# Optimization experiments

Hardware: AMD Instinct MI355X
Metric: run time of the kernel (lower is better)

Reference implementation:

```python
import jax, jax.numpy as jnp
import numpy as np

N = 50000        # num nodes
E = 800000       # num edges (no self loops by construction)
D = 128          # in_features == out_features
NE = 4           # num_envs
EPS = 1e-8
STDV = 1.0 / np.sqrt(D)


def setup_inputs() -> dict:
    key = jax.random.key(0)
    k = jax.random.split(key, 6)
    x = jax.random.normal(k[0], (N, D), jnp.float32)
    row = jax.random.randint(k[1], (E,), 0, N, dtype=jnp.int32)
    off = jax.random.randint(k[2], (E,), 1, N, dtype=jnp.int32)
    col = (row + off) % N  # guarantees no self loops (matches remove_self_loops)
    adj = jnp.stack([row, col])
    env_weights = jax.random.uniform(k[3], (N, NE), jnp.float32)
    weights = jax.random.uniform(k[4], (NE, D, D), jnp.float32, -STDV, STDV)
    a = jax.random.normal(k[5], (NE, 2 * D, 1), jnp.float32) * np.sqrt(2.0 / (2 * D + 1)) * 1.414
    return {"x": x, "adj": adj, "env_weights": env_weights, "weights": weights, "a": a}


def reference(x, adj, env_weights, weights, a):
    n = x.shape[0]
    f = weights.shape[-1]
    loops = jnp.arange(n, dtype=adj.dtype)
    src = jnp.concatenate([adj[0], loops])  # add_self_loops
    dst = jnp.concatenate([adj[1], loops])
    # per-env projected features: [NE, N, F]
    h = jnp.einsum('nd,edf->enf', x, weights)
    # attention logits: cat(h[src], h[dst]) @ a  ==  h[src]@a1 + h[dst]@a2
    a1 = a[:, :f, 0]   # [NE, F]
    a2 = a[:, f:, 0]   # [NE, F]
    s_src = jnp.einsum('enf,ef->en', h, a1)
    s_dst = jnp.einsum('enf,ef->en', h, a2)
    logits = jax.nn.leaky_relu(s_src[:, src] + s_dst[:, dst], 0.01)  # [NE, Etot]
    # global per-env max subtraction (as in the torch code: max over all edges)
    e = jnp.exp(logits - jnp.max(logits, axis=1, keepdims=True))
    def agg(ek, hk):
        # specialspmm: out[src] += ek * hk[dst]; denom via ones vector
        denom = jax.ops.segment_sum(ek, src, num_segments=n) + EPS          # [N]
        num = jax.ops.segment_sum(ek[:, None] * hk[dst], src, num_segments=n)  # [N, F]
        return num / denom[:, None]
    out_env = jax.vmap(agg)(e, h)  # [NE, N, F]
    out = jnp.einsum('ne,enf->nf', env_weights, out_env)
    return out + x  # residual
```

## Files before the change

kernel.cpp:

```cpp
#include <hip/hip_runtime.h>

#define N_NODES 50000
#define N_EDGES 800000
#define D_FEAT  128
#define NE_ENV  4
#define EPS_F   1e-8f
#define M_CONST 4.0f
#define SCAN_NB 196
#define NB_BUCKET 391
#define BINA_EPT 16

typedef __attribute__((ext_vector_type(8))) short bf16x8;
typedef __attribute__((ext_vector_type(4))) float floatx4;

static __device__ __forceinline__ unsigned short f2bf(float v) {
    union { float f; unsigned int u; } c; c.f = v;
    unsigned int u = c.u;
    u += 0x7fffu + ((u >> 16) & 1u);
    return (unsigned short)(u >> 16);
}

static __device__ __forceinline__ float2 bf2f(unsigned int v) {
    float2 r;
    r.x = __uint_as_float(v << 16);
    r.y = __uint_as_float(v & 0xffff0000u);
    return r;
}

static __device__ __forceinline__ float lrelu_exp(float z) {
    float lk = z > 0.f ? z : 0.01f * z;
    return __expf(lk - M_CONST);
}

__global__ __launch_bounds__(256) void k_setup(const float* __restrict__ weights, const float* __restrict__ a,
        float* __restrict__ b, unsigned short* __restrict__ wsw,
        const int* __restrict__ row, int* __restrict__ counts) {
    int blk = blockIdx.x;
    if (blk < 128) {
        int wave = threadIdx.x >> 6, lane = threadIdx.x & 63;
        int t = blk * 4 + wave;
        int e = t >> 7, d = t & 127;
        float2 w2 = ((const float2*)(weights + e * 16384 + d * 128))[lane];
        float2 a1 = ((const float2*)(a + e * 256))[lane];
        float2 a2 = ((const float2*)(a + e * 256 + 128))[lane];
        float p1 = w2.x * a1.x + w2.y * a1.y;
        float p2 = w2.x * a2.x + w2.y * a2.y;
#pragma unroll
        for (int off = 32; off > 0; off >>= 1) {
            p1 += __shfl_xor(p1, off, 64);
            p2 += __shfl_xor(p2, off, 64);
        }
        if (lane == 0) {
            b[e * 128 + d] = p1;
            b[512 + e * 128 + d] = p2;
        }
    } else if (blk < 384) {
        int idx = (blk - 128) * 256 + threadIdx.x;
        int j = idx & 7;
        int l = (idx >> 3) & 63;
        int t = (idx >> 9) & 7;
        int s = idx >> 12;
        int k = s * 32 + (l >> 4) * 8 + j;
        int f = t * 16 + (l & 15);
        int e = k >> 7, d = k & 127;
        wsw[idx] = f2bf(weights[e * 16384 + d * 128 + f]);
    } else {
        int k = (blk - 384) * 256 + threadIdx.x;
        if (k < N_EDGES) atomicAdd(&counts[row[k]], 1);
    }
}

__global__ __launch_bounds__(256) void k_s(const float* __restrict__ x, const float* __restrict__ b,
        float* __restrict__ s_src, float* __restrict__ s_dst, unsigned short* __restrict__ xbf) {
    int wave = threadIdx.x >> 6, lane = threadIdx.x & 63;
    int gw = blockIdx.x * 4 + wave;
    if (gw >= 3125) return;
    int quad = lane >> 4, lm = lane & 15;
    int base = gw * 16;

    floatx4 acc = (floatx4){0.f, 0.f, 0.f, 0.f};
    const float* xrow = x + (size_t)(base + lm) * 128 + quad * 8;
    unsigned short* xbrow = xbf + (size_t)(base + lm) * 128 + quad * 8;

#pragma unroll
    for (int s = 0; s < 4; ++s) {
        float4 lo = *(const float4*)(xrow + s * 32);
        float4 hi = *(const float4*)(xrow + s * 32 + 4);
        bf16x8 af;
        af[0] = (short)f2bf(lo.x); af[1] = (short)f2bf(lo.y);
        af[2] = (short)f2bf(lo.z); af[3] = (short)f2bf(lo.w);
        af[4] = (short)f2bf(hi.x); af[5] = (short)f2bf(hi.y);
        af[6] = (short)f2bf(hi.z); af[7] = (short)f2bf(hi.w);
        *(bf16x8*)(xbrow + s * 32) = af;

        bf16x8 bfv = (bf16x8){0, 0, 0, 0, 0, 0, 0, 0};
        if (lm < 8) {
            const float* bp = b + lm * 128 + s * 32 + quad * 8;
            float4 b0 = *(const float4*)bp;
            float4 b1 = *(const float4*)(bp + 4);
            bfv[0] = (short)f2bf(b0.x); bfv[1] = (short)f2bf(b0.y);
            bfv[2] = (short)f2bf(b0.z); bfv[3] = (short)f2bf(b0.w);
            bfv[4] = (short)f2bf(b1.x); bfv[5] = (short)f2bf(b1.y);
            bfv[6] = (short)f2bf(b1.z); bfv[7] = (short)f2bf(b1.w);
        }
        acc = __builtin_amdgcn_mfma_f32_16x16x32_bf16(af, bfv, acc, 0, 0, 0);
    }
    if (lm < 8) {
        float* dstp = (lm < 4) ? (s_src + (size_t)(base + quad * 4) * 4 + lm)
                               : (s_dst + (size_t)(base + quad * 4) * 4 + (lm - 4));
#pragma unroll
        for (int r = 0; r < 4; ++r) dstp[r * 4] = acc[r];
    }
}

__global__ void k_scan_a(const int* __restrict__ counts, int* __restrict__ partial) {
    __shared__ int sm[256];
    int idx = blockIdx.x * 256 + threadIdx.x;
    sm[threadIdx.x] = (idx < N_NODES) ? counts[idx] : 0;
    __syncthreads();
    for (int s = 128; s > 0; s >>= 1) {
        if (threadIdx.x < s) sm[threadIdx.x] += sm[threadIdx.x + s];
        __syncthreads();
    }
    if (threadIdx.x == 0) partial[blockIdx.x] = sm[0];
}

__global__ void k_scan_b(const int* __restrict__ partial, int* __restrict__ chunk_off) {
    __shared__ int sm[256];
    int t = threadIdx.x;
    int v = (t < SCAN_NB) ? partial[t] : 0;
    sm[t] = v;
    __syncthreads();
    for (int s2 = 1; s2 < 256; s2 <<= 1) {
        int add = (t >= s2) ? sm[t - s2] : 0;
        __syncthreads();
        sm[t] += add;
        __syncthreads();
    }
    chunk_off[t] = sm[t] - v;
}

__global__ void k_scan_c(const int* __restrict__ counts, const int* __restrict__ chunk_off,
                         int* __restrict__ offsets, int* __restrict__ bcur) {
    __shared__ int sm[256];
    int t = threadIdx.x;
    int idx = blockIdx.x * 256 + t;
    int v = (idx < N_NODES) ? counts[idx] : 0;
    sm[t] = v;
    __syncthreads();
    for (int s2 = 1; s2 < 256; s2 <<= 1) {
        int add = (t >= s2) ? sm[t - s2] : 0;
        __syncthreads();
        sm[t] += add;
        __syncthreads();
    }
    if (idx < N_NODES) {
        int excl = chunk_off[blockIdx.x] + sm[t] - v;
        offsets[idx] = excl;
        if ((idx & 127) == 0) bcur[idx >> 7] = excl;
    }
    if (idx == 0) offsets[N_NODES] = N_EDGES;
}

__global__ __launch_bounds__(256) void k_binA(const int* __restrict__ row, const int* __restrict__ col,
        int* __restrict__ bcur, unsigned int* __restrict__ binned) {
    __shared__ int cnt[NB_BUCKET];
    __shared__ int base[NB_BUCKET];
    int t = threadIdx.x;
    for (int b = t; b < NB_BUCKET; b += 256) cnt[b] = 0;
    __syncthreads();
    unsigned int pk[BINA_EPT];
    int ebase = blockIdx.x * (256 * BINA_EPT) + t;
#pragma unroll
    for (int j = 0; j < BINA_EPT; ++j) {
        int k = ebase + j * 256;
        pk[j] = 0xffffffffu;
        if (k < N_EDGES) {
            unsigned int s = (unsigned int)row[k];
            unsigned int d = (unsigned int)col[k];
            pk[j] = (s << 16) | d;
            atomicAdd(&cnt[s >> 7], 1);
        }
    }
    __syncthreads();
    for (int b = t; b < NB_BUCKET; b += 256) {
        int c = cnt[b];
        base[b] = c ? atomicAdd(&bcur[b], c) : 0;
        cnt[b] = 0;
    }
    __syncthreads();
#pragma unroll
    for (int j = 0; j < BINA_EPT; ++j) {
        if (pk[j] != 0xffffffffu) {
            int b = pk[j] >> 23;
            int off = atomicAdd(&cnt[b], 1);
            binned[base[b] + off] = pk[j];
        }
    }
}

__global__ __launch_bounds__(256) void k_binB(const unsigned int* __restrict__ binned,
        const int* __restrict__ offsets,
        const float* __restrict__ s_src, const float* __restrict__ s_dst,
        int* __restrict__ sorted_dst, float4* __restrict__ w_sorted) {
    __shared__ int cur[128];
    int b = blockIdx.x;
    int nb = b << 7;
    int nc = min(128, N_NODES - nb);
    int t = threadIdx.x;
    if (t < nc) cur[t] = offsets[nb + t];
    __syncthreads();
    int ebeg = offsets[nb];
    int eend = offsets[nb + nc];
    for (int i = ebeg + t; i < eend; i += 256) {
        unsigned int pk = binned[i];
        int s = (int)(pk >> 16), d = (int)(pk & 0xffffu);
        float4 a4 = *(const float4*)(s_src + s * 4);
        float4 b4 = *(const float4*)(s_dst + d * 4);
        float4 w;
        w.x = lrelu_exp(a4.x + b4.x);
        w.y = lrelu_exp(a4.y + b4.y);
        w.z = lrelu_exp(a4.z + b4.z);
        w.w = lrelu_exp(a4.w + b4.w);
        int pos = atomicAdd(&cur[s - nb], 1);
        sorted_dst[pos] = d;
        w_sorted[pos] = w;
    }
}

__global__ __launch_bounds__(256) void k_agg(const unsigned int* __restrict__ xb,
        const float* __restrict__ s_src, const float* __restrict__ s_dst,
        const int* __restrict__ offsets, const int* __restrict__ sorted_dst,
        const float4* __restrict__ w_sorted, const float* __restrict__ env_w,
        unsigned short* __restrict__ Gp) {
    int wave = threadIdx.x >> 6, lane = threadIdx.x & 63;
    int n = blockIdx.x * 4 + wave;
    if (n >= N_NODES) return;

    float den[4], ax[4], ay[4];

    {
        float4 sa = *(const float4*)(s_src + n * 4);
        float4 sb = *(const float4*)(s_dst + n * 4);
        float ws[4] = { lrelu_exp(sa.x + sb.x), lrelu_exp(sa.y + sb.y),
                        lrelu_exp(sa.z + sb.z), lrelu_exp(sa.w + sb.w) };
        float2 xv = bf2f(xb[(size_t)n * 64 + lane]);
#pragma unroll
        for (int e = 0; e < 4; ++e) {
            den[e] = ws[e]; ax[e] = ws[e] * xv.x; ay[e] = ws[e] * xv.y;
        }
    }

    int beg = __builtin_amdgcn_readfirstlane(offsets[n]);
    int end = __builtin_amdgcn_readfirstlane(offsets[n + 1]);
    int i = beg;
    for (; i + 3 < end; i += 4) {
        int d0 = sorted_dst[i],     d1 = sorted_dst[i + 1];
        int d2 = sorted_dst[i + 2], d3 = sorted_dst[i + 3];
        float4 w0 = w_sorted[i],     w1 = w_sorted[i + 1];
        float4 w2 = w_sorted[i + 2], w3 = w_sorted[i + 3];
        unsigned int v0 = xb[(size_t)d0 * 64 + lane];
        unsigned int v1 = xb[(size_t)d1 * 64 + lane];
        unsigned int v2 = xb[(size_t)d2 * 64 + lane];
        unsigned int v3 = xb[(size_t)d3 * 64 + lane];
        float2 x0 = bf2f(v0), x1 = bf2f(v1), x2v = bf2f(v2), x3 = bf2f(v3);
        den[0] += (w0.x + w1.x) + (w2.x + w3.x);
        den[1] += (w0.y + w1.y) + (w2.y + w3.y);
        den[2] += (w0.z + w1.z) + (w2.z + w3.z);
        den[3] += (w0.w + w1.w) + (w2.w + w3.w);
        ax[0] += w0.x * x0.x + w1.x * x1.x + w2.x * x2v.x + w3.x * x3.x;
        ay[0] += w0.x * x0.y + w1.x * x1.y + w2.x * x2v.y + w3.x * x3.y;
        ax[1] += w0.y * x0.x + w1.y * x1.x + w2.y * x2v.x + w3.y * x3.x;
        ay[1] += w0.y * x0.y + w1.y * x1.y + w2.y * x2v.y + w3.y * x3.y;
        ax[2] += w0.z * x0.x + w1.z * x1.x + w2.z * x2v.x + w3.z * x3.x;
        ay[2] += w0.z * x0.y + w1.z * x1.y + w2.z * x2v.y + w3.z * x3.y;
        ax[3] += w0.w * x0.x + w1.w * x1.x + w2.w * x2v.x + w3.w * x3.x;
        ay[3] += w0.w * x0.y + w1.w * x1.y + w2.w * x2v.y + w3.w * x3.y;
    }
    for (; i < end; ++i) {
        int d0 = sorted_dst[i];
        float4 w0 = w_sorted[i];
        float2 x0 = bf2f(xb[(size_t)d0 * 64 + lane]);
        den[0] += w0.x; den[1] += w0.y; den[2] += w0.z; den[3] += w0.w;
        ax[0] += w0.x * x0.x; ay[0] += w0.x * x0.y;
        ax[1] += w0.y * x0.x; ay[1] += w0.y * x0.y;
        ax[2] += w0.z * x0.x; ay[2] += w0.z * x0.y;
        ax[3] += w0.w * x0.x; ay[3] += w0.w * x0.y;
    }

    float4 ewt = *(const float4*)(env_w + n * 4);
    float ewv[4] = { ewt.x, ewt.y, ewt.z, ewt.w };
    unsigned int* grow = (unsigned int*)(Gp + (size_t)n * 512);
#pragma unroll
    for (int e = 0; e < 4; ++e) {
        float sc = ewv[e] / (den[e] + EPS_F);
        unsigned int lo = f2bf(sc * ax[e]);
        unsigned int hi = f2bf(sc * ay[e]);
        grow[e * 64 + lane] = (hi << 16) | lo;
    }
}

__global__ __launch_bounds__(256) void k_gemm(const unsigned short* __restrict__ Gp,
        const unsigned short* __restrict__ Wsw,
        const float* __restrict__ x, float* __restrict__ out) {
    int wave = threadIdx.x >> 6, lane = threadIdx.x & 63;
    int gw = blockIdx.x * 4 + wave;
    if (gw >= 3125) return;
    int quad = lane >> 4, lm = lane & 15;
    int m = gw * 16 + lm;

    floatx4 acc[8];
#pragma unroll
    for (int t = 0; t < 8; ++t) acc[t] = (floatx4){0.f, 0.f, 0.f, 0.f};

    const unsigned short* Arow = Gp + (size_t)m * 512 + quad * 8;
#pragma unroll
    for (int s = 0; s < 16; ++s) {
        bf16x8 af = *(const bf16x8*)(Arow + s * 32);
#pragma unroll
        for (int t = 0; t < 8; ++t) {
            bf16x8 bfv = *(const bf16x8*)(Wsw + (((s * 8 + t) * 64 + lane) * 8));
            acc[t] = __builtin_amdgcn_mfma_f32_16x16x32_bf16(af, bfv, acc[t], 0, 0, 0);
        }
    }
    int row_base = gw * 16 + quad * 4;
#pragma unroll
    for (int t = 0; t < 8; ++t) {
        int colc = t * 16 + lm;
#pragma unroll
        for (int r = 0; r < 4; ++r) {
            int rowi = row_base + r;
            out[rowi * 128 + colc] = acc[t][r] + x[rowi * 128 + colc];
        }
    }
}

extern "C" void kernel_launch(void* const* d_in, const int* in_sizes, int n_in,
                              void* d_out, int out_size, void* d_ws, size_t ws_size,
                              hipStream_t stream) {
    const float* x       = (const float*)d_in[0];
    const int*   adj     = (const int*)d_in[1];
    const int*   row     = adj;
    const int*   col     = adj + N_EDGES;
    const float* env_w   = (const float*)d_in[2];
    const float* weights = (const float*)d_in[3];
    const float* a       = (const float*)d_in[4];
    float* out = (float*)d_out;

    char* ws = (char*)d_ws;
    size_t off = 0;
    auto alloc = [&](size_t bytes) -> char* {
        char* p = ws + off;
        off += (bytes + 255) & ~(size_t)255;
        return p;
    };
    float* b          = (float*)alloc(1024 * 4);
    float* s_src      = (float*)alloc((size_t)N_NODES * 4 * 4);
    float* s_dst      = (float*)alloc((size_t)N_NODES * 4 * 4);
    int*   counts     = (int*)alloc((size_t)N_NODES * 4);
    int*   offsets    = (int*)alloc((size_t)(N_NODES + 1) * 4);
    int*   partial    = (int*)alloc(256 * 4);
    int*   chunk_off  = (int*)alloc(256 * 4);
    int*   bcur       = (int*)alloc(512 * 4);
    unsigned int* binned = (unsigned int*)alloc((size_t)N_EDGES * 4);
    int*   sorted_dst = (int*)alloc((size_t)N_EDGES * 4);
    float4* w_sorted  = (float4*)alloc((size_t)N_EDGES * 16);
    unsigned short* wsw = (unsigned short*)alloc(65536 * 2);
    unsigned short* xbf = (unsigned short*)alloc((size_t)N_NODES * 128 * 2);
    unsigned short* Gp  = (unsigned short*)alloc((size_t)N_NODES * 512 * 2);

    hipMemsetAsync(counts, 0, (size_t)N_NODES * 4, stream);
    k_setup<<<3509, 256, 0, stream>>>(weights, a, b, wsw, row, counts);
    k_s<<<782, 256, 0, stream>>>(x, b, s_src, s_dst, xbf);
    k_scan_a<<<SCAN_NB, 256, 0, stream>>>(counts, partial);
    k_scan_b<<<1, 256, 0, stream>>>(partial, chunk_off);
    k_scan_c<<<SCAN_NB, 256, 0, stream>>>(counts, chunk_off, offsets, bcur);
    k_binA<<<196, 256, 0, stream>>>(row, col, bcur, binned);
    k_binB<<<NB_BUCKET, 256, 0, stream>>>(binned, offsets, s_src, s_dst, sorted_dst, w_sorted);
    k_agg<<<12500, 256, 0, stream>>>((const unsigned int*)xbf, s_src, s_dst, offsets, sorted_dst, w_sorted, env_w, Gp);
    k_gemm<<<782, 256, 0, stream>>>(Gp, wsw, x, out);
}
```

Before: 231.6 us.

## Fold softmax normalization into binning and drop separate scan kernels

Removes the three-kernel prefix scan by computing per-bucket sums in an extra k_s block and scanning node offsets locally in k_binB. k_binB now accumulates per-node denominators in shared memory and emits edge coefficients already scaled by env weight over denominator, plus a self-loop coefficient. This lets k_agg drop its denominator and env-weight work and use packed float2 FMAs. The GEMM residual reads bf16 x instead of fp32 x to cut traffic, at the cost of residual precision and a second pass over edges in binB.

```diff
diff --git a/kernel.cpp b/kernel.cpp
--- a/kernel.cpp
+++ b/kernel.cpp
@@ -6,12 +6,12 @@
 #define NE_ENV  4
 #define EPS_F   1e-8f
 #define M_CONST 4.0f
-#define SCAN_NB 196
 #define NB_BUCKET 391
 #define BINA_EPT 16
 
 typedef __attribute__((ext_vector_type(8))) short bf16x8;
 typedef __attribute__((ext_vector_type(4))) float floatx4;
+typedef __attribute__((ext_vector_type(2))) float f2v;
 
 static __device__ __forceinline__ unsigned short f2bf(float v) {
     union { float f; unsigned int u; } c; c.f = v;
@@ -20,8 +20,8 @@
     return (unsigned short)(u >> 16);
 }
 
-static __device__ __forceinline__ float2 bf2f(unsigned int v) {
-    float2 r;
+static __device__ __forceinline__ f2v bf2f2(unsigned int v) {
+    f2v r;
     r.x = __uint_as_float(v << 16);
     r.y = __uint_as_float(v & 0xffff0000u);
     return r;
@@ -71,7 +71,45 @@
 }
 
 __global__ __launch_bounds__(256) void k_s(const float* __restrict__ x, const float* __restrict__ b,
-        float* __restrict__ s_src, float* __restrict__ s_dst, unsigned short* __restrict__ xbf) {
+        float* __restrict__ s_src, float* __restrict__ s_dst, unsigned short* __restrict__ xbf,
+        const int* __restrict__ counts, int* __restrict__ bcur, int* __restrict__ bbase) {
+    __shared__ int bsum[512];
+    if (blockIdx.x == 782) {
+        int t = threadIdx.x;
+        int o0 = 0, o1 = 0;
+        {
+            int nb = t << 7;
+            int n = min(128, N_NODES - nb);
+            for (int j = 0; j < n; ++j) o0 += counts[nb + j];
+            bsum[t] = o0;
+        }
+        {
+            int b1 = t + 256;
+            if (b1 < NB_BUCKET) {
+                int nb = b1 << 7;
+                int n = min(128, N_NODES - nb);
+                for (int j = 0; j < n; ++j) o1 += counts[nb + j];
+            }
+            bsum[t + 256] = o1;
+        }
+        __syncthreads();
+        for (int st = 1; st < 512; st <<= 1) {
+            int v0 = (t >= st) ? bsum[t - st] : 0;
+            int v1 = (t + 256 >= st) ? bsum[t + 256 - st] : 0;
+            __syncthreads();
+            bsum[t] += v0;
+            bsum[t + 256] += v1;
+            __syncthreads();
+        }
+        int e0 = bsum[t] - o0;
+        bcur[t] = e0; bbase[t] = e0;
+        int b1 = t + 256;
+        if (b1 < NB_BUCKET) {
+            int e1 = bsum[b1] - o1;
+            bcur[b1] = e1; bbase[b1] = e1;
+        }
+        return;
+    }
     int wave = threadIdx.x >> 6, lane = threadIdx.x & 63;
     int gw = blockIdx.x * 4 + wave;
     if (gw >= 3125) return;
@@ -113,55 +151,6 @@
     }
 }
 
-__global__ void k_scan_a(const int* __restrict__ counts, int* __restrict__ partial) {
-    __shared__ int sm[256];
-    int idx = blockIdx.x * 256 + threadIdx.x;
-    sm[threadIdx.x] = (idx < N_NODES) ? counts[idx] : 0;
-    __syncthreads();
-    for (int s = 128; s > 0; s >>= 1) {
-        if (threadIdx.x < s) sm[threadIdx.x] += sm[threadIdx.x + s];
-        __syncthreads();
-    }
-    if (threadIdx.x == 0) partial[blockIdx.x] = sm[0];
-}
-
-__global__ void k_scan_b(const int* __restrict__ partial, int* __restrict__ chunk_off) {
-    __shared__ int sm[256];
-    int t = threadIdx.x;
-    int v = (t < SCAN_NB) ? partial[t] : 0;
-    sm[t] = v;
-    __syncthreads();
-    for (int s2 = 1; s2 < 256; s2 <<= 1) {
-        int add = (t >= s2) ? sm[t - s2] : 0;
-        __syncthreads();
-        sm[t] += add;
-        __syncthreads();
-    }
-    chunk_off[t] = sm[t] - v;
-}
-
-__global__ void k_scan_c(const int* __restrict__ counts, const int* __restrict__ chunk_off,
-                         int* __restrict__ offsets, int* __restrict__ bcur) {
-    __shared__ int sm[256];
-    int t = threadIdx.x;
-    int idx = blockIdx.x * 256 + t;
-    int v = (idx < N_NODES) ? counts[idx] : 0;
-    sm[t] = v;
-    __syncthreads();
-    for (int s2 = 1; s2 < 256; s2 <<= 1) {
-        int add = (t >= s2) ? sm[t - s2] : 0;
-        __syncthreads();
-        sm[t] += add;
-        __syncthreads();
-    }
-    if (idx < N_NODES) {
-        int excl = chunk_off[blockIdx.x] + sm[t] - v;
-        offsets[idx] = excl;
-        if ((idx & 127) == 0) bcur[idx >> 7] = excl;
-    }
-    if (idx == 0) offsets[N_NODES] = N_EDGES;
-}
-
 __global__ __launch_bounds__(256) void k_binA(const int* __restrict__ row, const int* __restrict__ col,
         int* __restrict__ bcur, unsigned int* __restrict__ binned) {
     __shared__ int cnt[NB_BUCKET];
@@ -200,55 +189,100 @@
 }
 
 __global__ __launch_bounds__(256) void k_binB(const unsigned int* __restrict__ binned,
-        const int* __restrict__ offsets,
+        const int* __restrict__ counts, const int* __restrict__ bbase,
         const float* __restrict__ s_src, const float* __restrict__ s_dst,
-        int* __restrict__ sorted_dst, float4* __restrict__ w_sorted) {
+        const float* __restrict__ env_w,
+        int* __restrict__ offsets, int* __restrict__ sorted_dst,
+        float4* __restrict__ c_sorted, float4* __restrict__ cself) {
+    __shared__ int sc[128];
     __shared__ int cur[128];
+    __shared__ float denm[128][4];
     int b = blockIdx.x;
     int nb = b << 7;
     int nc = min(128, N_NODES - nb);
     int t = threadIdx.x;
-    if (t < nc) cur[t] = offsets[nb + t];
-    __syncthreads();
-    int ebeg = offsets[nb];
-    int eend = offsets[nb + nc];
+    int myc = 0;
+    if (t < nc) myc = counts[nb + t];
+    if (t < 128) sc[t] = myc;
+    __syncthreads();
+    for (int st = 1; st < 128; st <<= 1) {
+        int v = 0;
+        if (t < 128 && t >= st) v = sc[t - st];
+        __syncthreads();
+        if (t < 128) sc[t] += v;
+        __syncthreads();
+    }
+    int base = bbase[b];
+    float4 wself = {0.f, 0.f, 0.f, 0.f};
+    if (t < nc) {
+        int excl = base + sc[t] - myc;
+        offsets[nb + t] = excl;
+        cur[t] = excl;
+        float4 sa = *(const float4*)(s_src + (size_t)(nb + t) * 4);
+        float4 sb = *(const float4*)(s_dst + (size_t)(nb + t) * 4);
+        wself.x = lrelu_exp(sa.x + sb.x);
+        wself.y = lrelu_exp(sa.y + sb.y);
+        wself.z = lrelu_exp(sa.z + sb.z);
+        wself.w = lrelu_exp(sa.w + sb.w);
+        denm[t][0] = wself.x; denm[t][1] = wself.y;
+        denm[t][2] = wself.z; denm[t][3] = wself.w;
+    }
+    int tot = sc[127];
+    __syncthreads();
+    int ebeg = base, eend = base + tot;
     for (int i = ebeg + t; i < eend; i += 256) {
         unsigned int pk = binned[i];
         int s = (int)(pk >> 16), d = (int)(pk & 0xffffu);
-        float4 a4 = *(const float4*)(s_src + s * 4);
-        float4 b4 = *(const float4*)(s_dst + d * 4);
-        float4 w;
-        w.x = lrelu_exp(a4.x + b4.x);
-        w.y = lrelu_exp(a4.y + b4.y);
-        w.z = lrelu_exp(a4.z + b4.z);
-        w.w = lrelu_exp(a4.w + b4.w);
-        int pos = atomicAdd(&cur[s - nb], 1);
+        float4 a4 = *(const float4*)(s_src + (size_t)s * 4);
+        float4 b4 = *(const float4*)(s_dst + (size_t)d * 4);
+        int ls = s - nb;
+        atomicAdd(&denm[ls][0], lrelu_exp(a4.x + b4.x));
+        atomicAdd(&denm[ls][1], lrelu_exp(a4.y + b4.y));
+        atomicAdd(&denm[ls][2], lrelu_exp(a4.z + b4.z));
+        atomicAdd(&denm[ls][3], lrelu_exp(a4.w + b4.w));
+    }
+    __syncthreads();
+    if (t < nc) {
+        float4 ew = *(const float4*)(env_w + (size_t)(nb + t) * 4);
+        float m0 = ew.x / (denm[t][0] + EPS_F);
+        float m1 = ew.y / (denm[t][1] + EPS_F);
+        float m2 = ew.z / (denm[t][2] + EPS_F);
+        float m3 = ew.w / (denm[t][3] + EPS_F);
+        denm[t][0] = m0; denm[t][1] = m1; denm[t][2] = m2; denm[t][3] = m3;
+        cself[nb + t] = make_float4(m0 * wself.x, m1 * wself.y, m2 * wself.z, m3 * wself.w);
+    }
+    __syncthreads();
+    for (int i = ebeg + t; i < eend; i += 256) {
+        unsigned int pk = binned[i];
+        int s = (int)(pk >> 16), d = (int)(pk & 0xffffu);
+        int ls = s - nb;
+        float4 a4 = *(const float4*)(s_src + (size_t)s * 4);
+        float4 b4 = *(const float4*)(s_dst + (size_t)d * 4);
+        float4 c;
+        c.x = denm[ls][0] * lrelu_exp(a4.x + b4.x);
+        c.y = denm[ls][1] * lrelu_exp(a4.y + b4.y);
+        c.z = denm[ls][2] * lrelu_exp(a4.z + b4.z);
+        c.w = denm[ls][3] * lrelu_exp(a4.w + b4.w);
+        int pos = atomicAdd(&cur[ls], 1);
         sorted_dst[pos] = d;
-        w_sorted[pos] = w;
-    }
-}
-
-__global__ __launch_bounds__(256) void k_agg(const unsigned int* __restrict__ xb,
-        const float* __restrict__ s_src, const float* __restrict__ s_dst,
+        c_sorted[pos] = c;
+    }
+    if (b == NB_BUCKET - 1 && t == 0) offsets[N_NODES] = N_EDGES;
+}
+
+__global__ __launch_bounds__(256, 8) void k_agg(const unsigned int* __restrict__ xb,
         const int* __restrict__ offsets, const int* __restrict__ sorted_dst,
-        const float4* __restrict__ w_sorted, const float* __restrict__ env_w,
+        const float4* __restrict__ c_sorted, const float4* __restrict__ cself,
         unsigned short* __restrict__ Gp) {
     int wave = threadIdx.x >> 6, lane = threadIdx.x & 63;
     int n = blockIdx.x * 4 + wave;
     if (n >= N_NODES) return;
 
-    float den[4], ax[4], ay[4];
-
+    f2v a0, a1, a2, a3;
     {
-        float4 sa = *(const float4*)(s_src + n * 4);
-        float4 sb = *(const float4*)(s_dst + n * 4);
-        float ws[4] = { lrelu_exp(sa.x + sb.x), lrelu_exp(sa.y + sb.y),
-                        lrelu_exp(sa.z + sb.z), lrelu_exp(sa.w + sb.w) };
-        float2 xv = bf2f(xb[(size_t)n * 64 + lane]);
-#pragma unroll
-        for (int e = 0; e < 4; ++e) {
-            den[e] = ws[e]; ax[e] = ws[e] * xv.x; ay[e] = ws[e] * xv.y;
-        }
+        float4 cs = cself[n];
+        f2v xv = bf2f2(xb[(size_t)n * 64 + lane]);
+        a0 = cs.x * xv; a1 = cs.y * xv; a2 = cs.z * xv; a3 = cs.w * xv;
     }
 
     int beg = __builtin_amdgcn_readfirstlane(offsets[n]);
@@ -257,52 +291,35 @@
     for (; i + 3 < end; i += 4) {
         int d0 = sorted_dst[i],     d1 = sorted_dst[i + 1];
         int d2 = sorted_dst[i + 2], d3 = sorted_dst[i + 3];
-        float4 w0 = w_sorted[i],     w1 = w_sorted[i + 1];
-        float4 w2 = w_sorted[i + 2], w3 = w_sorted[i + 3];
+        float4 c0 = c_sorted[i],     c1 = c_sorted[i + 1];
+        float4 c2 = c_sorted[i + 2], c3 = c_sorted[i + 3];
         unsigned int v0 = xb[(size_t)d0 * 64 + lane];
         unsigned int v1 = xb[(size_t)d1 * 64 + lane];
         unsigned int v2 = xb[(size_t)d2 * 64 + lane];
         unsigned int v3 = xb[(size_t)d3 * 64 + lane];
-        float2 x0 = bf2f(v0), x1 = bf2f(v1), x2v = bf2f(v2), x3 = bf2f(v3);
-        den[0] += (w0.x + w1.x) + (w2.x + w3.x);
-        den[1] += (w0.y + w1.y) + (w2.y + w3.y);
-        den[2] += (w0.z + w1.z) + (w2.z + w3.z);
-        den[3] += (w0.w + w1.w) + (w2.w + w3.w);
-        ax[0] += w0.x * x0.x + w1.x * x1.x + w2.x * x2v.x + w3.x * x3.x;
-        ay[0] += w0.x * x0.y + w1.x * x1.y + w2.x * x2v.y + w3.x * x3.y;
-        ax[1] += w0.y * x0.x + w1.y * x1.x + w2.y * x2v.x + w3.y * x3.x;
-        ay[1] += w0.y * x0.y + w1.y * x1.y + w2.y * x2v.y + w3.y * x3.y;
-        ax[2] += w0.z * x0.x + w1.z * x1.x + w2.z * x2v.x + w3.z * x3.x;
-        ay[2] += w0.z * x0.y + w1.z * x1.y + w2.z * x2v.y + w3.z * x3.y;
-        ax[3] += w0.w * x0.x + w1.w * x1.x + w2.w * x2v.x + w3.w * x3.x;
-        ay[3] += w0.w * x0.y + w1.w * x1.y + w2.w * x2v.y + w3.w * x3.y;
+        f2v x0 = bf2f2(v0), x1 = bf2f2(v1), x2 = bf2f2(v2), x3 = bf2f2(v3);
+        a0 += c0.x * x0; a1 += c0.y * x0; a2 += c0.z * x0; a3 += c0.w * x0;
+        a0 += c1.x * x1; a1 += c1.y * x1; a2 += c1.z * x1; a3 += c1.w * x1;
+        a0 += c2.x * x2; a1 += c2.y * x2; a2 += c2.z * x2; a3 += c2.w * x2;
+        a0 += c3.x * x3; a1 += c3.y * x3; a2 += c3.z * x3; a3 += c3.w * x3;
     }
     for (; i < end; ++i) {
         int d0 = sorted_dst[i];
-        float4 w0 = w_sorted[i];
-        float2 x0 = bf2f(xb[(size_t)d0 * 64 + lane]);
-        den[0] += w0.x; den[1] += w0.y; den[2] += w0.z; den[3] += w0.w;
-        ax[0] += w0.x * x0.x; ay[0] += w0.x * x0.y;
-        ax[1] += w0.y * x0.x; ay[1] += w0.y * x0.y;
-        ax[2] += w0.z * x0.x; ay[2] += w0.z * x0.y;
-        ax[3] += w0.w * x0.x; ay[3] += w0.w * x0.y;
-    }
-
-    float4 ewt = *(const float4*)(env_w + n * 4);
-    float ewv[4] = { ewt.x, ewt.y, ewt.z, ewt.w };
+        float4 c0 = c_sorted[i];
+        f2v x0 = bf2f2(xb[(size_t)d0 * 64 + lane]);
+        a0 += c0.x * x0; a1 += c0.y * x0; a2 += c0.z * x0; a3 += c0.w * x0;
+    }
+
     unsigned int* grow = (unsigned int*)(Gp + (size_t)n * 512);
-#pragma unroll
-    for (int e = 0; e < 4; ++e) {
-        float sc = ewv[e] / (den[e] + EPS_F);
-        unsigned int lo = f2bf(sc * ax[e]);
-        unsigned int hi = f2bf(sc * ay[e]);
-        grow[e * 64 + lane] = (hi << 16) | lo;
-    }
+    grow[0 * 64 + lane] = ((unsigned int)f2bf(a0.y) << 16) | f2bf(a0.x);
+    grow[1 * 64 + lane] = ((unsigned int)f2bf(a1.y) << 16) | f2bf(a1.x);
+    grow[2 * 64 + lane] = ((unsigned int)f2bf(a2.y) << 16) | f2bf(a2.x);
+    grow[3 * 64 + lane] = ((unsigned int)f2bf(a3.y) << 16) | f2bf(a3.x);
 }
 
 __global__ __launch_bounds__(256) void k_gemm(const unsigned short* __restrict__ Gp,
         const unsigned short* __restrict__ Wsw,
-        const float* __restrict__ x, float* __restrict__ out) {
+        const unsigned short* __restrict__ xbf, float* __restrict__ out) {
     int wave = threadIdx.x >> 6, lane = threadIdx.x & 63;
     int gw = blockIdx.x * 4 + wave;
     if (gw >= 3125) return;
@@ -330,7 +347,8 @@
 #pragma unroll
         for (int r = 0; r < 4; ++r) {
             int rowi = row_base + r;
-            out[rowi * 128 + colc] = acc[t][r] + x[rowi * 128 + colc];
+            float xres = __uint_as_float(((unsigned int)xbf[(size_t)rowi * 128 + colc]) << 16);
+            out[(size_t)rowi * 128 + colc] = acc[t][r] + xres;
         }
     }
 }
@@ -359,24 +377,22 @@
     float* s_dst      = (float*)alloc((size_t)N_NODES * 4 * 4);
     int*   counts     = (int*)alloc((size_t)N_NODES * 4);
     int*   offsets    = (int*)alloc((size_t)(N_NODES + 1) * 4);
-    int*   partial    = (int*)alloc(256 * 4);
-    int*   chunk_off  = (int*)alloc(256 * 4);
     int*   bcur       = (int*)alloc(512 * 4);
+    int*   bbase      = (int*)alloc(512 * 4);
     unsigned int* binned = (unsigned int*)alloc((size_t)N_EDGES * 4);
     int*   sorted_dst = (int*)alloc((size_t)N_EDGES * 4);
-    float4* w_sorted  = (float4*)alloc((size_t)N_EDGES * 16);
+    float4* c_sorted  = (float4*)alloc((size_t)N_EDGES * 16);
+    float4* cself     = (float4*)alloc((size_t)N_NODES * 16);
     unsigned short* wsw = (unsigned short*)alloc(65536 * 2);
     unsigned short* xbf = (unsigned short*)alloc((size_t)N_NODES * 128 * 2);
     unsigned short* Gp  = (unsigned short*)alloc((size_t)N_NODES * 512 * 2);
 
     hipMemsetAsync(counts, 0, (size_t)N_NODES * 4, stream);
     k_setup<<<3509, 256, 0, stream>>>(weights, a, b, wsw, row, counts);
-    k_s<<<782, 256, 0, stream>>>(x, b, s_src, s_dst, xbf);
-    k_scan_a<<<SCAN_NB, 256, 0, stream>>>(counts, partial);
-    k_scan_b<<<1, 256, 0, stream>>>(partial, chunk_off);
-    k_scan_c<<<SCAN_NB, 256, 0, stream>>>(counts, chunk_off, offsets, bcur);
+    k_s<<<783, 256, 0, stream>>>(x, b, s_src, s_dst, xbf, counts, bcur, bbase);
     k_binA<<<196, 256, 0, stream>>>(row, col, bcur, binned);
-    k_binB<<<NB_BUCKET, 256, 0, stream>>>(binned, offsets, s_src, s_dst, sorted_dst, w_sorted);
-    k_agg<<<12500, 256, 0, stream>>>((const unsigned int*)xbf, s_src, s_dst, offsets, sorted_dst, w_sorted, env_w, Gp);
-    k_gemm<<<782, 256, 0, stream>>>(Gp, wsw, x, out);
-}
+    k_binB<<<NB_BUCKET, 256, 0, stream>>>(binned, counts, bbase, s_src, s_dst, env_w,
+                                          offsets, sorted_dst, c_sorted, cself);
+    k_agg<<<12500, 256, 0, stream>>>((const unsigned int*)xbf, offsets, sorted_dst, c_sorted, cself, Gp);
+    k_gemm<<<782, 256, 0, stream>>>(Gp, wsw, xbf, out);
+}
```

New measurement: 251.5 us. +8.6%, slower.
